# Kernel tuning notes

Hardware: AMD Instinct MI355X
Metric: run time of the kernel (lower is better)

## Reference

```python
import jax, jax.numpy as jnp
import numpy as np

M = 256                # grid cells per dimension
HINV2 = float(M * M)   # 1/h^2 with h = 1/m
CG_TOL = 1e-6
CG_MAXITER = 300


def _stencil_coeffs(alpha):
    """Edge diffusion coefficients of the 5-point stencil.

    alpha: (m+1, m+1) vertex field. Returns (diag, K_left, K_right, K_bottom, K_top),
    each (m, m), matching Solver2d._set_matrix_values / apply_operator.
    """
    m = alpha.shape[-1] - 1
    j = jnp.arange(m)[:, None]
    k = jnp.arange(m)[None, :]
    K_left = jnp.exp(0.5 * (alpha[:-1, :-1] + alpha[:-1, 1:]))
    K_right = jnp.where(j < m - 1, jnp.exp(0.5 * (alpha[1:, :-1] + alpha[1:, 1:])), 0.0)
    K_bottom = jnp.where(k > 0, jnp.exp(0.5 * (alpha[:-1, :-1] + alpha[1:, :-1])), 0.0)
    K_top = jnp.where(k < m - 1, jnp.exp(0.5 * (alpha[:-1, 1:] + alpha[1:, 1:])), 0.0)
    # Dirichlet boundary at j==0 contributes an extra K_left on the diagonal
    diag = K_left + K_right + K_bottom + K_top + jnp.where(j == 0, K_left, 0.0)
    return diag, K_left, K_right, K_bottom, K_top


def _apply_op(alpha, u):
    """Matrix-free A(alpha) @ u, u: (m, m). Same math as Solver2d.apply_operator."""
    diag, K_left, K_right, K_bottom, K_top = _stencil_coeffs(alpha)
    u_jm1 = jnp.pad(u[:-1, :], ((1, 0), (0, 0)))  # u[j-1,k], zero row at j=0 (j>0 guard)
    u_jp1 = jnp.pad(u[1:, :], ((0, 1), (0, 0)))   # u[j+1,k]
    u_km1 = jnp.pad(u[:, :-1], ((0, 0), (1, 0)))  # u[j,k-1]
    u_kp1 = jnp.pad(u[:, 1:], ((0, 0), (0, 1)))   # u[j,k+1]
    return HINV2 * (diag * u - K_left * u_jm1 - K_right * u_jp1
                    - K_bottom * u_km1 - K_top * u_kp1)


def _solve_one(alpha, f):
    """Solve A(alpha) u = f with CG (A is SPD), replacing the PETSc KSP solve."""
    u, _ = jax.scipy.sparse.linalg.cg(lambda v: _apply_op(alpha, v), f,
                                      tol=CG_TOL, maxiter=CG_MAXITER)
    return u


def setup_inputs() -> dict:
    key = jax.random.key(0)
    k1, k2 = jax.random.split(key)
    # mild log-diffusivity so exp(alpha) stays well conditioned
    alpha = 0.5 * jax.random.normal(k1, (64, M + 1, M + 1), dtype=jnp.float32)
    f_rhs = jax.random.normal(k2, (M, M), dtype=jnp.float32)
    return {"alpha": alpha, "f_rhs": f_rhs}


def reference(alpha, f_rhs):
    # batched alpha (B, m+1, m+1), shared RHS (m, m) -> u (B, m, m)
    return jax.vmap(_solve_one, in_axes=(0, None))(alpha, f_rhs)
```

## Files before the change

### kernel.cpp

```cpp
#include <hip/hip_runtime.h>
#include <math.h>

#define TPB     128
#define NBATCH  64
#define SPB     16
#define NBLK    (NBATCH*SPB)
#define SROWS   16
#define MM      256
#define AN      257
#define NITER   300
#define NIT1    (NITER+1)
#define SARR    (NBATCH*NIT1)
#define RS      264
#define CO(k)   ((k) + ((k) >> 5))

typedef float v4f __attribute__((ext_vector_type(4)));

__device__ __forceinline__ float mulf(float a, float b) {
  float d; asm("v_mul_f32 %0, %1, %2" : "=v"(d) : "v"(a), "v"(b)); return d;
}
__device__ __forceinline__ float addf(float a, float b) {
  float d; asm("v_add_f32 %0, %1, %2" : "=v"(d) : "v"(a), "v"(b)); return d;
}
__device__ __forceinline__ float subf(float a, float b) {
  float d; asm("v_sub_f32 %0, %1, %2" : "=v"(d) : "v"(a), "v"(b)); return d;
}
__device__ __forceinline__ float fmacf(float acc, float x, float y) {
  asm("v_fmac_f32 %0, %1, %2" : "+v"(acc) : "v"(x), "v"(y)); return acc;
}

__device__ __forceinline__ v4f ld4c(const float* p) {
  v4f r;
  asm volatile("global_load_dwordx4 %0, %1, off sc0 sc1" : "=v"(r) : "v"(p) : "memory");
  return r;
}
__device__ __forceinline__ void st4c(float* p, v4f v) {
  asm volatile("global_store_dwordx4 %0, %1, off sc0 sc1" :: "v"(p), "v"(v) : "memory");
}
__device__ __forceinline__ void vmdrain()  { asm volatile("s_waitcnt vmcnt(0)" ::: "memory"); }
__device__ __forceinline__ void drain_all(){ asm volatile("s_waitcnt vmcnt(0) lgkmcnt(0)" ::: "memory"); }

#define ALD_F(p)    __hip_atomic_load((p),  __ATOMIC_RELAXED, __HIP_MEMORY_SCOPE_AGENT)
#define AST_F(p,v)  __hip_atomic_store((p), (v), __ATOMIC_RELAXED, __HIP_MEMORY_SCOPE_AGENT)
#define ALD_I(p)    __hip_atomic_load((p),  __ATOMIC_RELAXED, __HIP_MEMORY_SCOPE_AGENT)
#define AST_I(p,v)  __hip_atomic_store((p), (v), __ATOMIC_RELAXED, __HIP_MEMORY_SCOPE_AGENT)
#define AADD_I(p)   __hip_atomic_fetch_add((p), 1, __ATOMIC_RELAXED, __HIP_MEMORY_SCOPE_AGENT)

__global__ void init_ws_kernel(int* __restrict__ z, int n) {
  int i = blockIdx.x * blockDim.x + threadIdx.x;
  if (i < n) z[i] = 0;
}

__device__ __forceinline__ void waitEq(int* p, int target) {
  int tries = 0;
  while (ALD_I(p) < target) {
    __builtin_amdgcn_s_sleep(2);
    if (++tries > (1 << 22)) break;
  }
}

#define W2_FMA16 \
    if (lw < 16) { \
      _Pragma("unroll") \
      for (int cj = 0; cj < 16; ++cj) \
        acc = fmacf(acc, sW[cj * 16 + lw], sW[256 + cj * 16 + lw]); \
    }

#define W2_STEP(D) { \
    asm volatile("s_waitcnt vmcnt(14)" ::: "memory"); \
    *(v4f*)&sW[wix]       = xq[D]; \
    *(v4f*)&sW[256 + wix] = yq[D]; \
    asm volatile("s_waitcnt lgkmcnt(0)" ::: "memory"); \
    xq[D] = ld4c(xp + (size_t)(P0 + (D) + 8) * 512); \
    yq[D] = ld4c(yp + (size_t)(P0 + (D) + 8) * 512); \
    W2_FMA16 \
    asm volatile("s_waitcnt lgkmcnt(0)" ::: "memory"); }

#define W2_TAIL(D, VM) { \
    asm volatile("s_waitcnt vmcnt(" #VM ")" ::: "memory"); \
    *(v4f*)&sW[wix]       = xq[D]; \
    *(v4f*)&sW[256 + wix] = yq[D]; \
    asm volatile("s_waitcnt lgkmcnt(0)" ::: "memory"); \
    W2_FMA16 \
    asm volatile("s_waitcnt lgkmcnt(0)" ::: "memory"); }

__device__ float dot2w(const float* __restrict__ X, const float* __restrict__ Y,
                       float* __restrict__ sDot, float* __restrict__ sAcc, int tid) {
  const int lw  = tid & 63;
  const int wid = tid >> 6;
  float* sW = sDot + wid * 512;
  const int off = (lw >> 2) * 32 + (lw & 3) * 4 + wid * 16;
  const int wix = (lw >> 2) * 16 + (lw & 3) * 4;
  const float* xp = X + off;
  const float* yp = Y + off;
  v4f xq[8], yq[8];
  #pragma unroll
  for (int d = 0; d < 8; ++d) {
    xq[d] = ld4c(xp + (size_t)d * 512);
    yq[d] = ld4c(yp + (size_t)d * 512);
  }
  float acc = 0.0f;
  #pragma unroll 1
  for (int g = 0; g < 15; ++g) {
    const int P0 = g * 8;
    W2_STEP(0) W2_STEP(1) W2_STEP(2) W2_STEP(3)
    W2_STEP(4) W2_STEP(5) W2_STEP(6) W2_STEP(7)
  }
  W2_TAIL(0, 14) W2_TAIL(1, 12) W2_TAIL(2, 10) W2_TAIL(3, 8)
  W2_TAIL(4, 6)  W2_TAIL(5, 4)  W2_TAIL(6, 2)  W2_TAIL(7, 0)

  if (lw < 16) sAcc[wid * 16 + lw] = acc;
  __syncthreads();
  float d0[32];
  #pragma unroll
  for (int o = 0; o < 32; ++o) d0[o] = sAcc[o];
  float C[8];
  #pragma unroll
  for (int l = 0; l < 8; ++l)
    C[l] = addf(addf(d0[l], d0[8 + l]), addf(d0[16 + l], d0[24 + l]));
  float D[4];
  #pragma unroll
  for (int l = 0; l < 4; ++l) D[l] = addf(C[l], C[l + 4]);
  float res = addf(addf(D[0], D[1]), addf(D[2], D[3]));
  __syncthreads();
  return res;
}

#define SQ_FMA16 \
    if (lw < 16) { \
      _Pragma("unroll") \
      for (int cj = 0; cj < 16; ++cj) { \
        float xv = sW[cj * 16 + lw]; \
        acc = fmacf(acc, xv, xv); \
      } \
    }

#define SQ_STEP(D) { \
    asm volatile("s_waitcnt vmcnt(15)" ::: "memory"); \
    *(v4f*)&sW[wix] = xq[D]; \
    asm volatile("s_waitcnt lgkmcnt(0)" ::: "memory"); \
    xq[D] = ld4c(xp + (size_t)(P0 + (D) + 16) * 512); \
    SQ_FMA16 \
    asm volatile("s_waitcnt lgkmcnt(0)" ::: "memory"); }

#define SQ_TAIL(D, VM) { \
    asm volatile("s_waitcnt vmcnt(" #VM ")" ::: "memory"); \
    *(v4f*)&sW[wix] = xq[D]; \
    asm volatile("s_waitcnt lgkmcnt(0)" ::: "memory"); \
    SQ_FMA16 \
    asm volatile("s_waitcnt lgkmcnt(0)" ::: "memory"); }

__device__ float dotSq(const float* __restrict__ X,
                       float* __restrict__ sDot, float* __restrict__ sAcc, int tid) {
  const int lw  = tid & 63;
  const int wid = tid >> 6;
  float* sW = sDot + wid * 512;
  const int off = (lw >> 2) * 32 + (lw & 3) * 4 + wid * 16;
  const int wix = (lw >> 2) * 16 + (lw & 3) * 4;
  const float* xp = X + off;
  v4f xq[16];
  #pragma unroll
  for (int d = 0; d < 16; ++d) xq[d] = ld4c(xp + (size_t)d * 512);
  float acc = 0.0f;
  #pragma unroll 1
  for (int g = 0; g < 7; ++g) {
    const int P0 = g * 16;
    SQ_STEP(0)  SQ_STEP(1)  SQ_STEP(2)  SQ_STEP(3)
    SQ_STEP(4)  SQ_STEP(5)  SQ_STEP(6)  SQ_STEP(7)
    SQ_STEP(8)  SQ_STEP(9)  SQ_STEP(10) SQ_STEP(11)
    SQ_STEP(12) SQ_STEP(13) SQ_STEP(14) SQ_STEP(15)
  }
  SQ_TAIL(0, 15)  SQ_TAIL(1, 14)  SQ_TAIL(2, 13)  SQ_TAIL(3, 12)
  SQ_TAIL(4, 11)  SQ_TAIL(5, 10)  SQ_TAIL(6, 9)   SQ_TAIL(7, 8)
  SQ_TAIL(8, 7)   SQ_TAIL(9, 6)   SQ_TAIL(10, 5)  SQ_TAIL(11, 4)
  SQ_TAIL(12, 3)  SQ_TAIL(13, 2)  SQ_TAIL(14, 1)  SQ_TAIL(15, 0)

  if (lw < 16) sAcc[wid * 16 + lw] = acc;
  __syncthreads();
  float d0[32];
  #pragma unroll
  for (int o = 0; o < 32; ++o) d0[o] = sAcc[o];
  float C[8];
  #pragma unroll
  for (int l = 0; l < 8; ++l)
    C[l] = addf(addf(d0[l], d0[8 + l]), addf(d0[16 + l], d0[24 + l]));
  float D[4];
  #pragma unroll
  for (int l = 0; l < 4; ++l) D[l] = addf(C[l], C[l + 4]);
  float res = addf(addf(D[0], D[1]), addf(D[2], D[3]));
  __syncthreads();
  return res;
}

__launch_bounds__(TPB, 2)
__global__ void cg_kernel(const float* __restrict__ alpha,
                          const float* __restrict__ frhs,
                          float* __restrict__ out,
                          int* __restrict__ Z,
                          float* __restrict__ av,
                          float* __restrict__ bv,
                          float* __restrict__ halo,
                          float* __restrict__ pbuf,
                          float* __restrict__ apbuf,
                          float* __restrict__ rbuf)
{
  __shared__ float sP[(SROWS + 2) * RS];
  __shared__ __align__(16) float sDot[1024];
  __shared__ float sAcc[32];

  int* cntP  = Z + 0 * SARR;
  int* cntA  = Z + 1 * SARR;
  int* cntB  = Z + 2 * SARR;
  int* flagA = Z + 3 * SARR;
  int* flagB = Z + 4 * SARR;

  const int tid  = threadIdx.x;
  const int bx   = blockIdx.x;
  const int b    = bx >> 4;
  const int s    = bx & 15;
  const int js   = s * SROWS;
  const int jloc = tid >> 3;
  const int k0   = (tid & 7) << 5;
  const int jg   = js + jloc;
  const int rowb = (jloc + 1) * RS;
  const int bNI  = b * NIT1;
  const size_t gbase = (size_t)b * (MM * MM) + (size_t)jg * MM + k0;

  float kl[32], kr[32], kbx[33], dg[32];
  {
    const float* r0 = alpha + (size_t)b * (AN * AN) + (size_t)jg * AN + k0;
    const float* r1 = r0 + AN;
    float a0[33], a1[33];
    #pragma unroll
    for (int i = 0; i < 33; ++i) { a0[i] = r0[i]; a1[i] = r1[i]; }
    #pragma unroll
    for (int i = 0; i < 33; ++i) kbx[i] = expf(0.5f * (a0[i] + a1[i]));
    #pragma unroll
    for (int i = 0; i < 32; ++i) {
      const int kg = k0 + i;
      float vkl = expf(0.5f * (a0[i] + a0[i + 1]));
      float vkr = (jg < MM - 1) ? expf(0.5f * (a1[i] + a1[i + 1])) : 0.0f;
      float vkb = (kg > 0)      ? kbx[i]     : 0.0f;
      float vkt = (kg < MM - 1) ? kbx[i + 1] : 0.0f;
      float d = ((vkl + vkr) + vkb) + vkt;
      if (jg == 0) d += vkl;
      kl[i] = vkl; kr[i] = vkr; dg[i] = d;
    }
  }

  float uu[32], rr[32], pp[32], Ap[32];
  {
    const float* fB = frhs + (size_t)jg * MM + k0;
    #pragma unroll
    for (int i = 0; i < 32; ++i) {
      float v = fB[i];
      uu[i] = 0.0f; rr[i] = v; pp[i] = v;
      sP[rowb + CO(k0 + i)] = v;
    }
    #pragma unroll
    for (int q = 0; q < 8; ++q) {
      v4f pv; pv[0] = pp[4*q]; pv[1] = pp[4*q+1]; pv[2] = pp[4*q+2]; pv[3] = pp[4*q+3];
      st4c(&pbuf[gbase + 4 * q], pv);
      st4c(&rbuf[gbase + 4 * q], pv);
    }
  }
  float* myhalo = halo + (size_t)bx * 512;
  if (jloc == 0) {
    #pragma unroll
    for (int q = 0; q < 8; ++q) {
      v4f hv; hv[0] = pp[4*q]; hv[1] = pp[4*q+1]; hv[2] = pp[4*q+2]; hv[3] = pp[4*q+3];
      st4c(&myhalo[k0 + 4 * q], hv);
    }
  }
  if (jloc == SROWS - 1) {
    #pragma unroll
    for (int q = 0; q < 8; ++q) {
      v4f hv; hv[0] = pp[4*q]; hv[1] = pp[4*q+1]; hv[2] = pp[4*q+2]; hv[3] = pp[4*q+3];
      st4c(&myhalo[256 + k0 + 4 * q], hv);
    }
  }
  drain_all();
  __syncthreads();
  if (tid == 0) AADD_I(&cntP[bNI + 0]);

  float gamma_red = 0.0f;

  for (int it = 1; it <= NITER; ++it) {
    if (tid == 0) waitEq(&cntP[bNI + it - 1], SPB);
    __syncthreads();
    if (jloc == 0) {
      if (s > 0) {
        float* nh = halo + (size_t)(bx - 1) * 512 + 256;
        v4f hv[8];
        #pragma unroll
        for (int q = 0; q < 8; ++q) hv[q] = ld4c(&nh[k0 + 4 * q]);
        vmdrain();
        #pragma unroll
        for (int q = 0; q < 8; ++q) {
          sP[CO(k0 + 4*q)]     = hv[q][0];
          sP[CO(k0 + 4*q + 1)] = hv[q][1];
          sP[CO(k0 + 4*q + 2)] = hv[q][2];
          sP[CO(k0 + 4*q + 3)] = hv[q][3];
        }
      } else {
        #pragma unroll
        for (int i = 0; i < 32; ++i) sP[CO(k0 + i)] = 0.0f;
      }
    }
    if (jloc == SROWS - 1) {
      if (s < SPB - 1) {
        float* nh = halo + (size_t)(bx + 1) * 512;
        v4f hv[8];
        #pragma unroll
        for (int q = 0; q < 8; ++q) hv[q] = ld4c(&nh[k0 + 4 * q]);
        vmdrain();
        #pragma unroll
        for (int q = 0; q < 8; ++q) {
          sP[(SROWS + 1) * RS + CO(k0 + 4*q)]     = hv[q][0];
          sP[(SROWS + 1) * RS + CO(k0 + 4*q + 1)] = hv[q][1];
          sP[(SROWS + 1) * RS + CO(k0 + 4*q + 2)] = hv[q][2];
          sP[(SROWS + 1) * RS + CO(k0 + 4*q + 3)] = hv[q][3];
        }
      } else {
        #pragma unroll
        for (int i = 0; i < 32; ++i) sP[(SROWS + 1) * RS + CO(k0 + i)] = 0.0f;
      }
    }
    __syncthreads();

    {
      v4f apv;
      #pragma unroll
      for (int i = 0; i < 32; ++i) {
        const int kg = k0 + i;
        float pc = pp[i];
        float pd = sP[rowb - RS + CO(kg)];
        float pu = sP[rowb + RS + CO(kg)];
        float pl = (i > 0) ? pp[i - 1]
                           : ((k0 > 0) ? sP[rowb + CO(k0 - 1)] : 0.0f);
        float pr = (i < 31) ? pp[i + 1]
                            : ((kg < MM - 1) ? sP[rowb + CO(k0 + 32)] : 0.0f);
        float vkb = (kg > 0)      ? kbx[i]     : 0.0f;
        float vkt = (kg < MM - 1) ? kbx[i + 1] : 0.0f;
        float t = mulf(dg[i], pc);
        t = subf(t, mulf(kl[i], pd));
        t = subf(t, mulf(kr[i], pu));
        t = subf(t, mulf(vkb, pl));
        t = subf(t, mulf(vkt, pr));
        float ap = mulf(65536.0f, t);
        Ap[i] = ap;
        apv[i & 3] = ap;
        if ((i & 3) == 3) st4c(&apbuf[gbase + (i - 3)], apv);
      }
    }
    drain_all();
    __syncthreads();
    if (tid == 0) AADD_I(&cntA[bNI + it]);

    if (s == 0) {
      if (tid == 0) waitEq(&cntA[bNI + it], SPB);
      __syncthreads();
      const float* Pb  = pbuf  + (size_t)b * (MM * MM);
      const float* APb = apbuf + (size_t)b * (MM * MM);
      const float* Rb  = rbuf  + (size_t)b * (MM * MM);
      if (it == 1) gamma_red = dotSq(Rb, sDot, sAcc, tid);
      float pap = dot2w(Pb, APb, sDot, sAcc, tid);
      if (tid == 0) {
        AST_F(&av[bNI + it], gamma_red / pap);
        vmdrain();
        AST_I(&flagA[bNI + it], 1);
      }
    }

    if (tid == 0) waitEq(&flagA[bNI + it], 1);
    __syncthreads();
    float alf = ALD_F(&av[bNI + it]);
    {
      v4f rv;
      #pragma unroll
      for (int i = 0; i < 32; ++i) {
        uu[i] = addf(uu[i], mulf(alf, pp[i]));
        rr[i] = subf(rr[i], mulf(alf, Ap[i]));
        rv[i & 3] = rr[i];
        if ((i & 3) == 3) st4c(&rbuf[gbase + (i - 3)], rv);
      }
    }
    drain_all();
    __syncthreads();
    if (tid == 0) AADD_I(&cntB[bNI + it]);

    if (s == 0) {
      if (tid == 0) waitEq(&cntB[bNI + it], SPB);
      __syncthreads();
      const float* Rb = rbuf + (size_t)b * (MM * MM);
      float g2 = dotSq(Rb, sDot, sAcc, tid);
      if (tid == 0) {
        AST_F(&bv[bNI + it], g2 / gamma_red);
        vmdrain();
        AST_I(&flagB[bNI + it], 1);
      }
      gamma_red = g2;
    }

    if (tid == 0) waitEq(&flagB[bNI + it], 1);
    __syncthreads();
    float bet = ALD_F(&bv[bNI + it]);
    {
      v4f pv;
      #pragma unroll
      for (int i = 0; i < 32; ++i) {
        float pn = addf(rr[i], mulf(bet, pp[i]));
        pp[i] = pn;
        sP[rowb + CO(k0 + i)] = pn;
        pv[i & 3] = pn;
        if ((i & 3) == 3) st4c(&pbuf[gbase + (i - 3)], pv);
      }
    }
    if (jloc == 0) {
      #pragma unroll
      for (int q = 0; q < 8; ++q) {
        v4f hv; hv[0] = pp[4*q]; hv[1] = pp[4*q+1]; hv[2] = pp[4*q+2]; hv[3] = pp[4*q+3];
        st4c(&myhalo[k0 + 4 * q], hv);
      }
    }
    if (jloc == SROWS - 1) {
      #pragma unroll
      for (int q = 0; q < 8; ++q) {
        v4f hv; hv[0] = pp[4*q]; hv[1] = pp[4*q+1]; hv[2] = pp[4*q+2]; hv[3] = pp[4*q+3];
        st4c(&myhalo[256 + k0 + 4 * q], hv);
      }
    }
    drain_all();
    __syncthreads();
    if (tid == 0) AADD_I(&cntP[bNI + it]);
  }

  float* oB = out + gbase;
  #pragma unroll
  for (int i = 0; i < 32; ++i) oB[i] = uu[i];
}

extern "C" void kernel_launch(void* const* d_in, const int* in_sizes, int n_in,
                              void* d_out, int out_size, void* d_ws, size_t ws_size,
                              hipStream_t stream) {
  const float* alpha = (const float*)d_in[0];
  const float* frhs  = (const float*)d_in[1];
  float* out = (float*)d_out;

  char* ws = (char*)d_ws;
  int*   Z    = (int*)ws;
  float* av   = (float*)(ws + (size_t)5 * SARR * 4);
  float* bv   = (float*)(ws + (size_t)6 * SARR * 4);
  size_t ZR   = ((size_t)7 * SARR * 4 + 4095) & ~(size_t)4095;
  float* halo  = (float*)(ws + ZR);
  float* pbuf  = (float*)(ws + ZR + (size_t)NBLK * 512 * 4);
  float* apbuf = pbuf  + (size_t)NBATCH * MM * MM;
  float* rbuf  = apbuf + (size_t)NBATCH * MM * MM;

  int nz = 5 * SARR;
  hipLaunchKernelGGL(init_ws_kernel, dim3((nz + 255) / 256), dim3(256), 0, stream,
                     Z, nz);
  hipLaunchKernelGGL(cg_kernel, dim3(NBLK), dim3(TPB), 0, stream,
                     alpha, frhs, out, Z, av, bv, halo, pbuf, apbuf, rbuf);
}
```

Baseline: 42.13 ms.

## Fuse residual-norm reduction into alpha phase to drop one grid barrier per CG iteration

The leader block now computes the next residual norm directly as ||r - alpha*Ap||^2 from the previous r and Ap buffers, right after computing alpha. This lets it publish alpha and beta together under one flag. The second cross-block counter/flag barrier per iteration, and its wait for every block to write the updated r, are removed. The cost is that the leader reads two full buffers instead of one for the norm. The norm is also taken from a recomputed residual rather than the one the blocks store, which can change rounding slightly.

```diff
diff --git a/kernel.cpp b/kernel.cpp
--- a/kernel.cpp
+++ b/kernel.cpp
@@ -174,6 +174,78 @@
   SQ_TAIL(4, 11)  SQ_TAIL(5, 10)  SQ_TAIL(6, 9)   SQ_TAIL(7, 8)
   SQ_TAIL(8, 7)   SQ_TAIL(9, 6)   SQ_TAIL(10, 5)  SQ_TAIL(11, 4)
   SQ_TAIL(12, 3)  SQ_TAIL(13, 2)  SQ_TAIL(14, 1)  SQ_TAIL(15, 0)
+
+  if (lw < 16) sAcc[wid * 16 + lw] = acc;
+  __syncthreads();
+  float d0[32];
+  #pragma unroll
+  for (int o = 0; o < 32; ++o) d0[o] = sAcc[o];
+  float C[8];
+  #pragma unroll
+  for (int l = 0; l < 8; ++l)
+    C[l] = addf(addf(d0[l], d0[8 + l]), addf(d0[16 + l], d0[24 + l]));
+  float D[4];
+  #pragma unroll
+  for (int l = 0; l < 4; ++l) D[l] = addf(C[l], C[l + 4]);
+  float res = addf(addf(D[0], D[1]), addf(D[2], D[3]));
+  __syncthreads();
+  return res;
+}
+
+#define RR_FMA16 \
+    if (lw < 16) { \
+      _Pragma("unroll") \
+      for (int cj = 0; cj < 16; ++cj) { \
+        float xv = sW[cj * 16 + lw]; \
+        float yv = sW[256 + cj * 16 + lw]; \
+        float rn = subf(xv, mulf(alfv, yv)); \
+        acc = fmacf(acc, rn, rn); \
+      } \
+    }
+
+#define RR_STEP(D) { \
+    asm volatile("s_waitcnt vmcnt(14)" ::: "memory"); \
+    *(v4f*)&sW[wix]       = xq[D]; \
+    *(v4f*)&sW[256 + wix] = yq[D]; \
+    asm volatile("s_waitcnt lgkmcnt(0)" ::: "memory"); \
+    xq[D] = ld4c(xp + (size_t)(P0 + (D) + 8) * 512); \
+    yq[D] = ld4c(yp + (size_t)(P0 + (D) + 8) * 512); \
+    RR_FMA16 \
+    asm volatile("s_waitcnt lgkmcnt(0)" ::: "memory"); }
+
+#define RR_TAIL(D, VM) { \
+    asm volatile("s_waitcnt vmcnt(" #VM ")" ::: "memory"); \
+    *(v4f*)&sW[wix]       = xq[D]; \
+    *(v4f*)&sW[256 + wix] = yq[D]; \
+    asm volatile("s_waitcnt lgkmcnt(0)" ::: "memory"); \
+    RR_FMA16 \
+    asm volatile("s_waitcnt lgkmcnt(0)" ::: "memory"); }
+
+__device__ float dotRR(const float* __restrict__ X, const float* __restrict__ Y,
+                       float alfv,
+                       float* __restrict__ sDot, float* __restrict__ sAcc, int tid) {
+  const int lw  = tid & 63;
+  const int wid = tid >> 6;
+  float* sW = sDot + wid * 512;
+  const int off = (lw >> 2) * 32 + (lw & 3) * 4 + wid * 16;
+  const int wix = (lw >> 2) * 16 + (lw & 3) * 4;
+  const float* xp = X + off;
+  const float* yp = Y + off;
+  v4f xq[8], yq[8];
+  #pragma unroll
+  for (int d = 0; d < 8; ++d) {
+    xq[d] = ld4c(xp + (size_t)d * 512);
+    yq[d] = ld4c(yp + (size_t)d * 512);
+  }
+  float acc = 0.0f;
+  #pragma unroll 1
+  for (int g = 0; g < 15; ++g) {
+    const int P0 = g * 8;
+    RR_STEP(0) RR_STEP(1) RR_STEP(2) RR_STEP(3)
+    RR_STEP(4) RR_STEP(5) RR_STEP(6) RR_STEP(7)
+  }
+  RR_TAIL(0, 14) RR_TAIL(1, 12) RR_TAIL(2, 10) RR_TAIL(3, 8)
+  RR_TAIL(4, 6)  RR_TAIL(5, 4)  RR_TAIL(6, 2)  RR_TAIL(7, 0)
 
   if (lw < 16) sAcc[wid * 16 + lw] = acc;
   __syncthreads();
@@ -210,9 +282,7 @@
 
   int* cntP  = Z + 0 * SARR;
   int* cntA  = Z + 1 * SARR;
-  int* cntB  = Z + 2 * SARR;
-  int* flagA = Z + 3 * SARR;
-  int* flagB = Z + 4 * SARR;
+  int* flg   = Z + 3 * SARR;
 
   const int tid  = threadIdx.x;
   const int bx   = blockIdx.x;
@@ -364,17 +434,22 @@
       const float* APb = apbuf + (size_t)b * (MM * MM);
       const float* Rb  = rbuf  + (size_t)b * (MM * MM);
       if (it == 1) gamma_red = dotSq(Rb, sDot, sAcc, tid);
-      float pap = dot2w(Pb, APb, sDot, sAcc, tid);
+      float pap  = dot2w(Pb, APb, sDot, sAcc, tid);
+      float alfr = gamma_red / pap;
+      float g2   = dotRR(Rb, APb, alfr, sDot, sAcc, tid);
       if (tid == 0) {
-        AST_F(&av[bNI + it], gamma_red / pap);
+        AST_F(&av[bNI + it], alfr);
+        AST_F(&bv[bNI + it], g2 / gamma_red);
         vmdrain();
-        AST_I(&flagA[bNI + it], 1);
-      }
-    }
-
-    if (tid == 0) waitEq(&flagA[bNI + it], 1);
+        AST_I(&flg[bNI + it], 1);
+      }
+      gamma_red = g2;
+    }
+
+    if (tid == 0) waitEq(&flg[bNI + it], 1);
     __syncthreads();
     float alf = ALD_F(&av[bNI + it]);
+    float bet = ALD_F(&bv[bNI + it]);
     {
       v4f rv;
       #pragma unroll
@@ -385,26 +460,6 @@
         if ((i & 3) == 3) st4c(&rbuf[gbase + (i - 3)], rv);
       }
     }
-    drain_all();
-    __syncthreads();
-    if (tid == 0) AADD_I(&cntB[bNI + it]);
-
-    if (s == 0) {
-      if (tid == 0) waitEq(&cntB[bNI + it], SPB);
-      __syncthreads();
-      const float* Rb = rbuf + (size_t)b * (MM * MM);
-      float g2 = dotSq(Rb, sDot, sAcc, tid);
-      if (tid == 0) {
-        AST_F(&bv[bNI + it], g2 / gamma_red);
-        vmdrain();
-        AST_I(&flagB[bNI + it], 1);
-      }
-      gamma_red = g2;
-    }
-
-    if (tid == 0) waitEq(&flagB[bNI + it], 1);
-    __syncthreads();
-    float bet = ALD_F(&bv[bNI + it]);
     {
       v4f pv;
       #pragma unroll
```

New measurement: 65.31 ms. +55.0%, slower.

## Store CG scratch vectors in wave-coalesced permuted layout for stores and dot loads

Applied to the files above, without the earlier changes.

The global scratch buffers for p, r and Ap change from a row-major layout to a per-wave interleaved layout. Each wave's float4 stores now cover consecutive 16-byte slots across lanes, so a store instruction touches contiguous memory instead of a lane-strided 128-byte pattern. The dot-product readers get matching QADDR address maths. Since only dot products read these buffers and the permutation is consistent, results stay the same up to reduction order, but correctness depends on writer and reader mappings agreeing exactly.

```diff
diff --git a/kernel.cpp b/kernel.cpp
--- a/kernel.cpp
+++ b/kernel.cpp
@@ -59,6 +59,8 @@
   }
 }
 
+#define QADDR(P) ((size_t)(((P) >> 2) << 11) + (size_t)(((P) & 3) << 6))
+
 #define W2_FMA16 \
     if (lw < 16) { \
       _Pragma("unroll") \
@@ -71,8 +73,8 @@
     *(v4f*)&sW[wix]       = xq[D]; \
     *(v4f*)&sW[256 + wix] = yq[D]; \
     asm volatile("s_waitcnt lgkmcnt(0)" ::: "memory"); \
-    xq[D] = ld4c(xp + (size_t)(P0 + (D) + 8) * 512); \
-    yq[D] = ld4c(yp + (size_t)(P0 + (D) + 8) * 512); \
+    xq[D] = ld4c(xp + QADDR(P0 + (D) + 8)); \
+    yq[D] = ld4c(yp + QADDR(P0 + (D) + 8)); \
     W2_FMA16 \
     asm volatile("s_waitcnt lgkmcnt(0)" ::: "memory"); }
 
@@ -89,15 +91,15 @@
   const int lw  = tid & 63;
   const int wid = tid >> 6;
   float* sW = sDot + wid * 512;
-  const int off = (lw >> 2) * 32 + (lw & 3) * 4 + wid * 16;
-  const int wix = (lw >> 2) * 16 + (lw & 3) * 4;
-  const float* xp = X + off;
-  const float* yp = Y + off;
+  const int offp = ((lw & 3) + wid * 4) * 256 + (lw >> 2) * 4;
+  const int wix  = (lw >> 2) * 16 + (lw & 3) * 4;
+  const float* xp = X + offp;
+  const float* yp = Y + offp;
   v4f xq[8], yq[8];
   #pragma unroll
   for (int d = 0; d < 8; ++d) {
-    xq[d] = ld4c(xp + (size_t)d * 512);
-    yq[d] = ld4c(yp + (size_t)d * 512);
+    xq[d] = ld4c(xp + QADDR(d));
+    yq[d] = ld4c(yp + QADDR(d));
   }
   float acc = 0.0f;
   #pragma unroll 1
@@ -139,7 +141,7 @@
     asm volatile("s_waitcnt vmcnt(15)" ::: "memory"); \
     *(v4f*)&sW[wix] = xq[D]; \
     asm volatile("s_waitcnt lgkmcnt(0)" ::: "memory"); \
-    xq[D] = ld4c(xp + (size_t)(P0 + (D) + 16) * 512); \
+    xq[D] = ld4c(xp + QADDR(P0 + (D) + 16)); \
     SQ_FMA16 \
     asm volatile("s_waitcnt lgkmcnt(0)" ::: "memory"); }
 
@@ -155,12 +157,12 @@
   const int lw  = tid & 63;
   const int wid = tid >> 6;
   float* sW = sDot + wid * 512;
-  const int off = (lw >> 2) * 32 + (lw & 3) * 4 + wid * 16;
-  const int wix = (lw >> 2) * 16 + (lw & 3) * 4;
-  const float* xp = X + off;
+  const int offp = ((lw & 3) + wid * 4) * 256 + (lw >> 2) * 4;
+  const int wix  = (lw >> 2) * 16 + (lw & 3) * 4;
+  const float* xp = X + offp;
   v4f xq[16];
   #pragma unroll
-  for (int d = 0; d < 16; ++d) xq[d] = ld4c(xp + (size_t)d * 512);
+  for (int d = 0; d < 16; ++d) xq[d] = ld4c(xp + QADDR(d));
   float acc = 0.0f;
   #pragma unroll 1
   for (int g = 0; g < 7; ++g) {
@@ -225,6 +227,8 @@
   const int rowb = (jloc + 1) * RS;
   const int bNI  = b * NIT1;
   const size_t gbase = (size_t)b * (MM * MM) + (size_t)jg * MM + k0;
+  const int lane = tid & 63;
+  const size_t wbase = (size_t)b * (MM * MM) + (size_t)(js + (tid >> 6) * 8) * MM;
 
   float kl[32], kr[32], kbx[33], dg[32];
   {
@@ -260,8 +264,8 @@
     #pragma unroll
     for (int q = 0; q < 8; ++q) {
       v4f pv; pv[0] = pp[4*q]; pv[1] = pp[4*q+1]; pv[2] = pp[4*q+2]; pv[3] = pp[4*q+3];
-      st4c(&pbuf[gbase + 4 * q], pv);
-      st4c(&rbuf[gbase + 4 * q], pv);
+      st4c(&pbuf[wbase + (size_t)((q * 64 + lane) << 2)], pv);
+      st4c(&rbuf[wbase + (size_t)((q * 64 + lane) << 2)], pv);
     }
   }
   float* myhalo = halo + (size_t)bx * 512;
@@ -350,7 +354,8 @@
         float ap = mulf(65536.0f, t);
         Ap[i] = ap;
         apv[i & 3] = ap;
-        if ((i & 3) == 3) st4c(&apbuf[gbase + (i - 3)], apv);
+        if ((i & 3) == 3)
+          st4c(&apbuf[wbase + (size_t)((((i >> 2) * 64) + lane) << 2)], apv);
       }
     }
     drain_all();
@@ -382,7 +387,8 @@
         uu[i] = addf(uu[i], mulf(alf, pp[i]));
         rr[i] = subf(rr[i], mulf(alf, Ap[i]));
         rv[i & 3] = rr[i];
-        if ((i & 3) == 3) st4c(&rbuf[gbase + (i - 3)], rv);
+        if ((i & 3) == 3)
+          st4c(&rbuf[wbase + (size_t)((((i >> 2) * 64) + lane) << 2)], rv);
       }
     }
     drain_all();
@@ -413,7 +419,8 @@
         pp[i] = pn;
         sP[rowb + CO(k0 + i)] = pn;
         pv[i & 3] = pn;
-        if ((i & 3) == 3) st4c(&pbuf[gbase + (i - 3)], pv);
+        if ((i & 3) == 3)
+          st4c(&pbuf[wbase + (size_t)((((i >> 2) * 64) + lane) << 2)], pv);
       }
     }
     if (jloc == 0) {
```

New measurement: 40.91 ms. 2.9% less time.
